# Kernel tuning notes

Hardware: AMD Instinct MI355X
Metric: run time of the kernel (lower is better)

The kernel has to match this reference:

```python
import jax, jax.numpy as jnp
import numpy as np

B, N, DEG = 128, 512, 8          # graphs, nodes per graph, avg degree
E = B * N * DEG                  # 524288 edges
F_IN, H1, H2, C = 128, 64, 128, 10
RATIO = 0.8
K = int(np.ceil(RATIO * N))      # TopKPooling keeps ceil(0.8*N)=410 nodes per graph


def setup_inputs() -> dict:
    key = jax.random.key(0)
    ks = jax.random.split(key, 10)
    n_nodes = B * N
    x = jax.random.normal(ks[0], (n_nodes, F_IN), dtype=jnp.float32)
    # random intra-graph edges, then offset node ids per graph
    src = jax.random.randint(ks[1], (B, N * DEG), 0, N)
    dst = jax.random.randint(ks[2], (B, N * DEG), 0, N)
    off = (jnp.arange(B) * N)[:, None]
    edge_index = jnp.stack([(src + off).reshape(-1), (dst + off).reshape(-1)]).astype(jnp.int64)
    batch = jnp.repeat(jnp.arange(B), N).astype(jnp.int64)
    s1 = 1.0 / np.sqrt(F_IN)
    s2 = 1.0 / np.sqrt(H1)
    s3 = 1.0 / np.sqrt(H2)
    return {
        "x": x,
        "edge_index": edge_index,
        "batch": batch,
        "W1": jax.random.uniform(ks[3], (F_IN, H1), jnp.float32, -s1, s1),
        "b1": jnp.zeros((H1,), jnp.float32),
        "W2": jax.random.uniform(ks[4], (H1, H2), jnp.float32, -s2, s2),
        "b2": jnp.zeros((H2,), jnp.float32),
        "pool_w": jax.random.uniform(ks[5], (H2,), jnp.float32, -s3, s3),
        "fc_W": jax.random.uniform(ks[6], (H2, C), jnp.float32, -s3, s3),
        "fc_b": jax.random.uniform(ks[7], (C,), jnp.float32, -s3, s3),
    }


def gcn_conv(x, W, b, src, dst, num_nodes):
    # PyG GCNConv: add self-loops, symmetric normalization, scatter-add aggregation
    loop = jnp.arange(num_nodes)
    src = jnp.concatenate([src, loop])
    dst = jnp.concatenate([dst, loop])
    deg = jax.ops.segment_sum(jnp.ones_like(src, dtype=x.dtype), dst, num_segments=num_nodes)
    dis = jnp.where(deg > 0, jax.lax.rsqrt(jnp.maximum(deg, 1.0)), 0.0)
    norm = dis[src] * dis[dst]                       # [E+N]
    h = x @ W                                        # transform first (smaller of the two in conv1)
    out = jax.ops.segment_sum(norm[:, None] * h[src], dst, num_segments=num_nodes)
    return out + b


def reference(x, edge_index, batch, W1, b1, W2, b2, pool_w, fc_W, fc_b):
    num_nodes = x.shape[0]
    src, dst = edge_index[0], edge_index[1]
    x = jax.nn.relu(gcn_conv(x, W1, b1, src, dst, num_nodes))
    x = jax.nn.relu(gcn_conv(x, W2, b2, src, dst, num_nodes))
    # TopKPooling: score = (x . w)/||w||, per-graph top-k on raw score, gate by tanh(score)
    score = (x @ pool_w) / jnp.linalg.norm(pool_w)   # [B*N]
    score_b = score.reshape(B, N)
    top_vals, top_idx = jax.lax.top_k(score_b, K)    # [B, K]
    x_b = x.reshape(B, N, H2)
    x_sel = jnp.take_along_axis(x_b, top_idx[:, :, None], axis=1)   # [B, K, H2]
    x_sel = x_sel * jnp.tanh(top_vals)[:, :, None]
    # global max pool over each (pooled) graph; pooled edge_index is unused downstream
    g = jnp.max(x_sel, axis=1)                        # [B, H2]
    logits = g @ fc_W + fc_b                          # [B, C]
    return jax.nn.log_softmax(logits, axis=1)
```

## Files before the change

kernel.cpp:

```cpp
#include <hip/hip_runtime.h>
#include <hip/hip_bf16.h>


#define BB 128
#define NN 512
#define NODES (BB*NN)
#define EE (BB*NN*8)
#define EDGPG (NN*8)
#define F_IN 128
#define H1 64
#define H2 128
#define NC 10
#define KSEL 410
#define EPG (NN*8 + NN)
#define TOT_ADJ (EE + NODES)

typedef unsigned short u16;
typedef unsigned int   u32;

static __device__ __forceinline__ float lo2f(u32 u){ return __uint_as_float(u << 16); }
static __device__ __forceinline__ float hi2f(u32 u){ return __uint_as_float(u & 0xffff0000u); }
static __device__ __forceinline__ u16 f2b(float f){
    __hip_bfloat16 h = __float2bfloat16(f);
    return *reinterpret_cast<u16*>(&h);
}
static __device__ __forceinline__ u32 packbf(float a, float b){
    return (u32)f2b(a) | ((u32)f2b(b) << 16);
}
static __device__ __forceinline__ void acc8(float* a, uint4 v){
    a[0] += lo2f(v.x); a[1] += hi2f(v.x);
    a[2] += lo2f(v.y); a[3] += hi2f(v.y);
    a[4] += lo2f(v.z); a[5] += hi2f(v.z);
    a[6] += lo2f(v.w); a[7] += hi2f(v.w);
}

static __device__ __forceinline__ bool ei_is_i64(const int* __restrict__ ei){
    return ((ei[1] | ei[3] | ei[5] | ei[7]) == 0);
}
static __device__ __forceinline__ int ld_src(const int* __restrict__ ei, int e, bool w64){
    return w64 ? ei[2*e] : ei[e];
}
static __device__ __forceinline__ int ld_dst(const int* __restrict__ ei, int e, bool w64){
    return w64 ? ei[2*(EE + e)] : ei[EE + e];
}

__global__ __launch_bounds__(512) void k_build(const int* __restrict__ ei,
                                               int* __restrict__ row_start,
                                               int* __restrict__ cnt_g,
                                               float* __restrict__ dis,
                                               int* __restrict__ adj){
    __shared__ int cnt[NN];
    __shared__ int sh[NN];
    __shared__ int cur[NN];
    __shared__ u16 ldst[EDGPG];
    bool w64 = ei_is_i64(ei);
    int b = blockIdx.x, t = threadIdx.x;
    cnt[t] = 0;
    __syncthreads();
    int e0 = b*EDGPG;
    for (int i = t; i < EDGPG; i += 512){
        int d = (ld_dst(ei, e0 + i, w64) - b*NN) & (NN - 1);
        ldst[i] = (u16)d;
        atomicAdd(&cnt[d], 1);
    }
    __syncthreads();
    int tot = cnt[t] + 1;
    sh[t] = tot;
    __syncthreads();
    for (int off = 1; off < NN; off <<= 1){
        int v = (t >= off) ? sh[t-off] : 0;
        __syncthreads();
        sh[t] += v;
        __syncthreads();
    }
    int rs_local = sh[t] - tot;
    row_start[b*NN + t] = b*EPG + rs_local;
    cnt_g[b*NN + t]     = tot - 1;
    dis[b*NN + t]       = rsqrtf((float)tot);
    cur[t] = rs_local;
    __syncthreads();
    {
        int p = atomicAdd(&cur[t], 1);
        adj[b*EPG + p] = b*NN + t;
    }
    for (int i = t; i < EDGPG; i += 512){
        int d = (int)ldst[i];
        int s = ld_src(ei, e0 + i, w64) & (NODES - 1);
        int p = atomicAdd(&cur[d], 1);
        adj[b*EPG + p] = s;
    }
}

#define G1NODES 64
#define XPAD 68
__global__ __launch_bounds__(256) void k_gemm1(const float* __restrict__ x,
                                               const float* __restrict__ W1,
                                               const float* __restrict__ dis,
                                               u32* __restrict__ h1u){
    __shared__ __align__(16) float Ws[64*H1];
    __shared__ __align__(16) float xs[G1NODES*XPAD];
    int t = threadIdx.x;
    int node0 = blockIdx.x*G1NODES;
    int tc = t & 15, tr = t >> 4;
    int j0 = tc*4, n0 = tr*4;
    float acc[4][4] = {};
    for (int half = 0; half < 2; ++half){
        const float4* Wv = (const float4*)(W1 + half*4096);
        for (int i = t; i < 1024; i += 256)
            *(float4*)&Ws[i*4] = Wv[i];
        for (int i = t; i < 1024; i += 256){
            int node = i >> 4, c = i & 15;
            float4 v = *(const float4*)(x + (size_t)(node0 + node)*F_IN + half*64 + c*4);
            *(float4*)&xs[node*XPAD + c*4] = v;
        }
        __syncthreads();
        #pragma unroll 2
        for (int k = 0; k < 64; k += 4){
            float4 xv0 = *(const float4*)&xs[(n0+0)*XPAD + k];
            float4 xv1 = *(const float4*)&xs[(n0+1)*XPAD + k];
            float4 xv2 = *(const float4*)&xs[(n0+2)*XPAD + k];
            float4 xv3 = *(const float4*)&xs[(n0+3)*XPAD + k];
            float xa0[4] = {xv0.x, xv0.y, xv0.z, xv0.w};
            float xa1[4] = {xv1.x, xv1.y, xv1.z, xv1.w};
            float xa2[4] = {xv2.x, xv2.y, xv2.z, xv2.w};
            float xa3[4] = {xv3.x, xv3.y, xv3.z, xv3.w};
            #pragma unroll
            for (int kk = 0; kk < 4; ++kk){
                float4 wv = *(const float4*)&Ws[(k+kk)*H1 + j0];
                acc[0][0] += xa0[kk]*wv.x; acc[0][1] += xa0[kk]*wv.y; acc[0][2] += xa0[kk]*wv.z; acc[0][3] += xa0[kk]*wv.w;
                acc[1][0] += xa1[kk]*wv.x; acc[1][1] += xa1[kk]*wv.y; acc[1][2] += xa1[kk]*wv.z; acc[1][3] += xa1[kk]*wv.w;
                acc[2][0] += xa2[kk]*wv.x; acc[2][1] += xa2[kk]*wv.y; acc[2][2] += xa2[kk]*wv.z; acc[2][3] += xa2[kk]*wv.w;
                acc[3][0] += xa3[kk]*wv.x; acc[3][1] += xa3[kk]*wv.y; acc[3][2] += xa3[kk]*wv.z; acc[3][3] += xa3[kk]*wv.w;
            }
        }
        __syncthreads();
    }
    #pragma unroll
    for (int i = 0; i < 4; ++i){
        float dn = dis[node0 + n0 + i];
        size_t base = (size_t)(node0 + n0 + i)*32 + tc*2;
        h1u[base]     = packbf(dn*acc[i][0], dn*acc[i][1]);
        h1u[base + 1] = packbf(dn*acc[i][2], dn*acc[i][3]);
    }
}

__global__ __launch_bounds__(256) void k_agg1(const uint4* __restrict__ h1v,
                                              const int* __restrict__ row_start,
                                              const int* __restrict__ cnt,
                                              const int* __restrict__ adj,
                                              const float* __restrict__ dis,
                                              const float4* __restrict__ b1v,
                                              uint4* __restrict__ a1v){
    int t = threadIdx.x;
    int node = blockIdx.x*32 + (t >> 3);
    int fl = t & 7;
    int rs = row_start[node];
    int deg = cnt[node] + 1; if (deg > EPG) deg = EPG;
    int pe = rs + deg;
    float a0[8] = {}, a1r[8] = {}, a2r[8] = {}, a3r[8] = {};
    int p = rs;
    for (; p + 4 <= pe; p += 4){
        int s0 = adj[p], s1 = adj[p+1], s2 = adj[p+2], s3 = adj[p+3];
        uint4 v0 = h1v[s0*8 + fl];
        uint4 v1 = h1v[s1*8 + fl];
        uint4 v2 = h1v[s2*8 + fl];
        uint4 v3 = h1v[s3*8 + fl];
        acc8(a0, v0); acc8(a1r, v1); acc8(a2r, v2); acc8(a3r, v3);
    }
    for (; p < pe; ++p){
        uint4 v = h1v[adj[p]*8 + fl];
        acc8(a0, v);
    }
    float r[8];
    #pragma unroll
    for (int j = 0; j < 8; ++j) r[j] = (a0[j] + a1r[j]) + (a2r[j] + a3r[j]);
    float dn = dis[node];
    float4 bA = b1v[2*fl], bB = b1v[2*fl+1];
    float w0 = dn*r[0] + bA.x; w0 = w0 > 0.f ? w0 : 0.f;
    float w1 = dn*r[1] + bA.y; w1 = w1 > 0.f ? w1 : 0.f;
    float w2 = dn*r[2] + bA.z; w2 = w2 > 0.f ? w2 : 0.f;
    float w3 = dn*r[3] + bA.w; w3 = w3 > 0.f ? w3 : 0.f;
    float w4 = dn*r[4] + bB.x; w4 = w4 > 0.f ? w4 : 0.f;
    float w5 = dn*r[5] + bB.y; w5 = w5 > 0.f ? w5 : 0.f;
    float w6 = dn*r[6] + bB.z; w6 = w6 > 0.f ? w6 : 0.f;
    float w7 = dn*r[7] + bB.w; w7 = w7 > 0.f ? w7 : 0.f;
    a1v[node*8 + fl] = make_uint4(packbf(dn*w0, dn*w1), packbf(dn*w2, dn*w3),
                                  packbf(dn*w4, dn*w5), packbf(dn*w6, dn*w7));
}

#define G2NODES 32
#define APAD 68
__global__ __launch_bounds__(256) void k_gemm2s(const uint4* __restrict__ a1v,
                                                const int* __restrict__ row_start,
                                                const int* __restrict__ cnt,
                                                const int* __restrict__ adj,
                                                const float* __restrict__ dis,
                                                const float* __restrict__ W2,
                                                const float* __restrict__ b2,
                                                const float* __restrict__ pw,
                                                u32* __restrict__ a2u,
                                                float* __restrict__ score){
    __shared__ __align__(16) float Ws[32*H2];
    __shared__ __align__(16) float as[G2NODES*APAD];
    __shared__ float pws[H2];
    int t = threadIdx.x;
    int node0 = blockIdx.x*G2NODES;
    if (t < H2) pws[t] = pw[t];
    {
        int fl = t & 7, nl = t >> 3;
        int node = node0 + nl;
        int rs = row_start[node];
        int deg = cnt[node] + 1; if (deg > EPG) deg = EPG;
        int pe = rs + deg;
        float a0[8] = {}, a1r[8] = {}, a2r[8] = {}, a3r[8] = {};
        int p = rs;
        for (; p + 4 <= pe; p += 4){
            int s0 = adj[p], s1 = adj[p+1], s2 = adj[p+2], s3 = adj[p+3];
            uint4 v0 = a1v[s0*8 + fl];
            uint4 v1 = a1v[s1*8 + fl];
            uint4 v2 = a1v[s2*8 + fl];
            uint4 v3 = a1v[s3*8 + fl];
            acc8(a0, v0); acc8(a1r, v1); acc8(a2r, v2); acc8(a3r, v3);
        }
        for (; p < pe; ++p){
            uint4 v = a1v[adj[p]*8 + fl];
            acc8(a0, v);
        }
        float dn = dis[node];
        float* dst = &as[nl*APAD + 8*fl];
        float r0 = dn*((a0[0] + a1r[0]) + (a2r[0] + a3r[0]));
        float r1 = dn*((a0[1] + a1r[1]) + (a2r[1] + a3r[1]));
        float r2 = dn*((a0[2] + a1r[2]) + (a2r[2] + a3r[2]));
        float r3 = dn*((a0[3] + a1r[3]) + (a2r[3] + a3r[3]));
        float r4 = dn*((a0[4] + a1r[4]) + (a2r[4] + a3r[4]));
        float r5 = dn*((a0[5] + a1r[5]) + (a2r[5] + a3r[5]));
        float r6 = dn*((a0[6] + a1r[6]) + (a2r[6] + a3r[6]));
        float r7 = dn*((a0[7] + a1r[7]) + (a2r[7] + a3r[7]));
        *(float4*)&dst[0] = make_float4(r0, r1, r2, r3);
        *(float4*)&dst[4] = make_float4(r4, r5, r6, r7);
    }
    int tc = t & 31, tr = t >> 5;
    int j0 = tc*4, n0 = tr*4;
    float acc[4][4] = {};
    for (int half = 0; half < 2; ++half){
        const float4* Wv = (const float4*)(W2 + half*4096);
        for (int i = t; i < 1024; i += 256)
            *(float4*)&Ws[i*4] = Wv[i];
        __syncthreads();
        int kb = half*32;
        #pragma unroll 2
        for (int k = 0; k < 32; k += 4){
            float4 xv0 = *(const float4*)&as[(n0+0)*APAD + kb + k];
            float4 xv1 = *(const float4*)&as[(n0+1)*APAD + kb + k];
            float4 xv2 = *(const float4*)&as[(n0+2)*APAD + kb + k];
            float4 xv3 = *(const float4*)&as[(n0+3)*APAD + kb + k];
            float xa0[4] = {xv0.x, xv0.y, xv0.z, xv0.w};
            float xa1[4] = {xv1.x, xv1.y, xv1.z, xv1.w};
            float xa2[4] = {xv2.x, xv2.y, xv2.z, xv2.w};
            float xa3[4] = {xv3.x, xv3.y, xv3.z, xv3.w};
            #pragma unroll
            for (int kk = 0; kk < 4; ++kk){
                float4 wv = *(const float4*)&Ws[(k+kk)*H2 + j0];
                acc[0][0] += xa0[kk]*wv.x; acc[0][1] += xa0[kk]*wv.y; acc[0][2] += xa0[kk]*wv.z; acc[0][3] += xa0[kk]*wv.w;
                acc[1][0] += xa1[kk]*wv.x; acc[1][1] += xa1[kk]*wv.y; acc[1][2] += xa1[kk]*wv.z; acc[1][3] += xa1[kk]*wv.w;
                acc[2][0] += xa2[kk]*wv.x; acc[2][1] += xa2[kk]*wv.y; acc[2][2] += xa2[kk]*wv.z; acc[2][3] += xa2[kk]*wv.w;
                acc[3][0] += xa3[kk]*wv.x; acc[3][1] += xa3[kk]*wv.y; acc[3][2] += xa3[kk]*wv.z; acc[3][3] += xa3[kk]*wv.w;
            }
        }
        __syncthreads();
    }
    float p0 = pws[j0], p1 = pws[j0+1], p2 = pws[j0+2], p3 = pws[j0+3];
    float bj0 = b2[j0], bj1 = b2[j0+1], bj2 = b2[j0+2], bj3 = b2[j0+3];
    #pragma unroll
    for (int i = 0; i < 4; ++i){
        float v0 = acc[i][0] + bj0; v0 = v0 > 0.f ? v0 : 0.f;
        float v1 = acc[i][1] + bj1; v1 = v1 > 0.f ? v1 : 0.f;
        float v2 = acc[i][2] + bj2; v2 = v2 > 0.f ? v2 : 0.f;
        float v3 = acc[i][3] + bj3; v3 = v3 > 0.f ? v3 : 0.f;
        size_t base = (size_t)(node0 + n0 + i)*64 + tc*2;
        a2u[base]     = packbf(v0, v1);
        a2u[base + 1] = packbf(v2, v3);
        float sp = v0*p0 + v1*p1 + v2*p2 + v3*p3;
        sp += __shfl_xor(sp, 16, 32);
        sp += __shfl_xor(sp,  8, 32);
        sp += __shfl_xor(sp,  4, 32);
        sp += __shfl_xor(sp,  2, 32);
        sp += __shfl_xor(sp,  1, 32);
        if (tc == 0) score[node0 + n0 + i] = sp;
    }
}

__global__ __launch_bounds__(512) void k_pool(const u32* __restrict__ a2u,
                                              const float* __restrict__ score,
                                              const float* __restrict__ pw,
                                              const float* __restrict__ fcW,
                                              const float* __restrict__ fcb,
                                              float* __restrict__ out){
    __shared__ float so[NN];
    __shared__ float ss[NN];
    __shared__ float th[NN];
    __shared__ float pm[32*H2];
    __shared__ float gl[H2];
    __shared__ float fws[H2*NC];
    __shared__ float lg[NC];
    __shared__ float red[3];
    int b = blockIdx.x, t = threadIdx.x;
    for (int i = t; i < H2*NC; i += 512) fws[i] = fcW[i];
    if (t < H2){ float v = pw[t]; gl[t] = v*v; }
    __syncthreads();
    if (t == 0){
        float s = 0.f;
        for (int i = 0; i < H2; ++i) s += gl[i];
        red[2] = rsqrtf(s);
    }
    __syncthreads();
    float pwinv = red[2];
    float sc = score[b*NN + t];
    so[t] = sc; ss[t] = sc; th[t] = tanhf(sc*pwinv);
    __syncthreads();
    for (int k = 2; k <= NN; k <<= 1){
        for (int j = k >> 1; j > 0; j >>= 1){
            int ixj = t ^ j;
            if (ixj > t){
                float a = ss[t], c = ss[ixj];
                bool desc = ((t & k) == 0);
                bool sw = desc ? (a < c) : (a > c);
                if (sw){ ss[t] = c; ss[ixj] = a; }
            }
            __syncthreads();
        }
    }
    float thresh = ss[KSEL-1];
    float mask_t = (so[t] >= thresh) ? 0.f : -INFINITY;
    __syncthreads();
    so[t] = mask_t;
    __syncthreads();
    int tc = t & 15, q = t >> 4;
    const uint4* ap = (const uint4*)(a2u + (size_t)b*NN*64);
    float m0 = -INFINITY, m1 = -INFINITY, m2 = -INFINITY, m3 = -INFINITY;
    float m4 = -INFINITY, m5 = -INFINITY, m6 = -INFINITY, m7 = -INFINITY;
    int nb = q*16;
    #pragma unroll 4
    for (int n = nb; n < nb + 16; ++n){
        uint4 v = ap[(size_t)n*16 + tc];
        float thn = th[n], son = so[n];
        m0 = fmaxf(m0, lo2f(v.x)*thn + son);
        m1 = fmaxf(m1, hi2f(v.x)*thn + son);
        m2 = fmaxf(m2, lo2f(v.y)*thn + son);
        m3 = fmaxf(m3, hi2f(v.y)*thn + son);
        m4 = fmaxf(m4, lo2f(v.z)*thn + son);
        m5 = fmaxf(m5, hi2f(v.z)*thn + son);
        m6 = fmaxf(m6, lo2f(v.w)*thn + son);
        m7 = fmaxf(m7, hi2f(v.w)*thn + son);
    }
    float* pmr = &pm[q*H2 + 8*tc];
    pmr[0] = m0; pmr[1] = m1; pmr[2] = m2; pmr[3] = m3;
    pmr[4] = m4; pmr[5] = m5; pmr[6] = m6; pmr[7] = m7;
    __syncthreads();
    if (t < H2){
        float g = pm[t];
        #pragma unroll
        for (int qq = 1; qq < 32; ++qq) g = fmaxf(g, pm[qq*H2 + t]);
        gl[t] = g;
    }
    __syncthreads();
    if (t < NC){
        float acc = fcb[t];
        for (int k2 = 0; k2 < H2; ++k2) acc += gl[k2]*fws[k2*NC + t];
        lg[t] = acc;
    }
    __syncthreads();
    if (t == 0){
        float mx = lg[0];
        for (int i = 1; i < NC; ++i) mx = fmaxf(mx, lg[i]);
        float s = 0.f;
        for (int i = 0; i < NC; ++i) s += expf(lg[i] - mx);
        red[0] = mx; red[1] = logf(s);
    }
    __syncthreads();
    if (t < NC) out[b*NC + t] = lg[t] - red[0] - red[1];
}

extern "C" void kernel_launch(void* const* d_in, const int* in_sizes, int n_in,
                              void* d_out, int out_size, void* d_ws, size_t ws_size,
                              hipStream_t stream) {
    const float* x   = (const float*)d_in[0];
    const int*   ei  = (const int*)d_in[1];
    const float* W1  = (const float*)d_in[3];
    const float* b1  = (const float*)d_in[4];
    const float* W2  = (const float*)d_in[5];
    const float* b2  = (const float*)d_in[6];
    const float* pw  = (const float*)d_in[7];
    const float* fcW = (const float*)d_in[8];
    const float* fcb = (const float*)d_in[9];

    char* ws = (char*)d_ws;
    int*   cnt       = (int*)(ws + 4096);
    int*   row_start = (int*)(ws + 266240);
    float* dis       = (float*)(ws + 528384);
    float* score     = (float*)(ws + 790528);
    int*   adj       = (int*)(ws + 1052672);
    u32*   h1u       = (u32*)(ws + 4194304);
    u32*   a1u       = (u32*)(ws + 12582912);
    u32*   a2u       = (u32*)(ws + 20971520);

    k_build<<<BB, 512, 0, stream>>>(ei, row_start, cnt, dis, adj);
    k_gemm1<<<NODES/G1NODES, 256, 0, stream>>>(x, W1, dis, h1u);
    k_agg1<<<NODES/32, 256, 0, stream>>>((const uint4*)h1u, row_start, cnt, adj, dis,
                                         (const float4*)b1, (uint4*)a1u);
    k_gemm2s<<<NODES/G2NODES, 256, 0, stream>>>((const uint4*)a1u, row_start, cnt, adj,
                                                dis, W2, b2, pw, a2u, score);
    k_pool<<<BB, 512, 0, stream>>>(a2u, score, pw, fcW, fcb, (float*)d_out);
}
```

Measured before the change: 176.3 us.

## Fuse graph build with GEMM1 and pooling into GEMM2 via last-block counter

Merges the CSR build and first GEMM into one launch: the GEMM blocks recompute per-node degree from edge destinations themselves, so they need not wait for the build. The pooling/top-k/classifier stage is folded into the second GEMM kernel; the last of the 16 blocks covering a graph, detected with an atomic done counter and threadfences, runs the pooling for that graph with 256 threads. This removes two kernel launches and their inter-kernel gaps, at the cost of redundant edge scans in GEMM1 blocks and a serialized tail for pooling.

```diff
diff --git a/kernel.cpp b/kernel.cpp
--- a/kernel.cpp
+++ b/kernel.cpp
@@ -44,89 +44,110 @@
     return w64 ? ei[2*(EE + e)] : ei[EE + e];
 }
 
-__global__ __launch_bounds__(512) void k_build(const int* __restrict__ ei,
-                                               int* __restrict__ row_start,
-                                               int* __restrict__ cnt_g,
-                                               float* __restrict__ dis,
-                                               int* __restrict__ adj){
-    __shared__ int cnt[NN];
-    __shared__ int sh[NN];
-    __shared__ int cur[NN];
-    __shared__ u16 ldst[EDGPG];
+#define G1NODES 128
+#define XPAD 68
+#define G1BLOCKS (NODES/G1NODES)
+
+union SM1 {
+    struct { int cnt[NN]; int sh[NN]; int cur[NN]; u16 ldst[EDGPG]; } b;
+    struct { float Ws[64*H1]; float xs[G1NODES*XPAD]; int degs[G1NODES]; } g;
+};
+
+__global__ __launch_bounds__(512) void k_build_gemm1(const int* __restrict__ ei,
+                                                     const float* __restrict__ x,
+                                                     const float* __restrict__ W1,
+                                                     int* __restrict__ row_start,
+                                                     int* __restrict__ cnt_g,
+                                                     float* __restrict__ dis,
+                                                     int* __restrict__ adj,
+                                                     u32* __restrict__ h1u,
+                                                     int* __restrict__ done){
+    __shared__ SM1 sm;
     bool w64 = ei_is_i64(ei);
-    int b = blockIdx.x, t = threadIdx.x;
-    cnt[t] = 0;
-    __syncthreads();
-    int e0 = b*EDGPG;
-    for (int i = t; i < EDGPG; i += 512){
-        int d = (ld_dst(ei, e0 + i, w64) - b*NN) & (NN - 1);
-        ldst[i] = (u16)d;
-        atomicAdd(&cnt[d], 1);
-    }
-    __syncthreads();
-    int tot = cnt[t] + 1;
-    sh[t] = tot;
-    __syncthreads();
-    for (int off = 1; off < NN; off <<= 1){
-        int v = (t >= off) ? sh[t-off] : 0;
-        __syncthreads();
-        sh[t] += v;
-        __syncthreads();
-    }
-    int rs_local = sh[t] - tot;
-    row_start[b*NN + t] = b*EPG + rs_local;
-    cnt_g[b*NN + t]     = tot - 1;
-    dis[b*NN + t]       = rsqrtf((float)tot);
-    cur[t] = rs_local;
-    __syncthreads();
-    {
-        int p = atomicAdd(&cur[t], 1);
-        adj[b*EPG + p] = b*NN + t;
-    }
-    for (int i = t; i < EDGPG; i += 512){
-        int d = (int)ldst[i];
-        int s = ld_src(ei, e0 + i, w64) & (NODES - 1);
-        int p = atomicAdd(&cur[d], 1);
-        adj[b*EPG + p] = s;
-    }
-}
-
-#define G1NODES 64
-#define XPAD 68
-__global__ __launch_bounds__(256) void k_gemm1(const float* __restrict__ x,
-                                               const float* __restrict__ W1,
-                                               const float* __restrict__ dis,
-                                               u32* __restrict__ h1u){
-    __shared__ __align__(16) float Ws[64*H1];
-    __shared__ __align__(16) float xs[G1NODES*XPAD];
     int t = threadIdx.x;
-    int node0 = blockIdx.x*G1NODES;
+
+    if (blockIdx.x < BB){
+        int b = blockIdx.x;
+        if (t == 0) done[b] = 0;
+        sm.b.cnt[t] = 0;
+        __syncthreads();
+        int e0 = b*EDGPG;
+        for (int i = t; i < EDGPG; i += 512){
+            int d = (ld_dst(ei, e0 + i, w64) - b*NN) & (NN - 1);
+            sm.b.ldst[i] = (u16)d;
+            atomicAdd(&sm.b.cnt[d], 1);
+        }
+        __syncthreads();
+        int tot = sm.b.cnt[t] + 1;
+        sm.b.sh[t] = tot;
+        __syncthreads();
+        for (int off = 1; off < NN; off <<= 1){
+            int v = (t >= off) ? sm.b.sh[t-off] : 0;
+            __syncthreads();
+            sm.b.sh[t] += v;
+            __syncthreads();
+        }
+        int rs_local = sm.b.sh[t] - tot;
+        row_start[b*NN + t] = b*EPG + rs_local;
+        cnt_g[b*NN + t]     = tot - 1;
+        dis[b*NN + t]       = rsqrtf((float)tot);
+        sm.b.cur[t] = rs_local;
+        __syncthreads();
+        {
+            int p = atomicAdd(&sm.b.cur[t], 1);
+            adj[b*EPG + p] = b*NN + t;
+        }
+        for (int i = t; i < EDGPG; i += 512){
+            int d = (int)sm.b.ldst[i];
+            int s = ld_src(ei, e0 + i, w64) & (NODES - 1);
+            int p = atomicAdd(&sm.b.cur[d], 1);
+            adj[b*EPG + p] = s;
+        }
+        return;
+    }
+
+    int gb = (int)blockIdx.x - BB;
+    int b  = gb >> 2;
+    int nloc0 = (gb & 3) * G1NODES;
+    int node0 = b*NN + nloc0;
     int tc = t & 15, tr = t >> 4;
     int j0 = tc*4, n0 = tr*4;
+
+    if (t < G1NODES) sm.g.degs[t] = 0;
+    __syncthreads();
+    {
+        int e0 = b*EDGPG;
+        for (int i = t; i < EDGPG; i += 512){
+            int d = (ld_dst(ei, e0 + i, w64) - b*NN) & (NN - 1);
+            unsigned r = (unsigned)(d - nloc0);
+            if (r < G1NODES) atomicAdd(&sm.g.degs[r], 1);
+        }
+    }
+
     float acc[4][4] = {};
     for (int half = 0; half < 2; ++half){
         const float4* Wv = (const float4*)(W1 + half*4096);
-        for (int i = t; i < 1024; i += 256)
-            *(float4*)&Ws[i*4] = Wv[i];
-        for (int i = t; i < 1024; i += 256){
+        for (int i = t; i < 1024; i += 512)
+            *(float4*)&sm.g.Ws[i*4] = Wv[i];
+        for (int i = t; i < 2048; i += 512){
             int node = i >> 4, c = i & 15;
             float4 v = *(const float4*)(x + (size_t)(node0 + node)*F_IN + half*64 + c*4);
-            *(float4*)&xs[node*XPAD + c*4] = v;
+            *(float4*)&sm.g.xs[node*XPAD + c*4] = v;
         }
         __syncthreads();
         #pragma unroll 2
         for (int k = 0; k < 64; k += 4){
-            float4 xv0 = *(const float4*)&xs[(n0+0)*XPAD + k];
-            float4 xv1 = *(const float4*)&xs[(n0+1)*XPAD + k];
-            float4 xv2 = *(const float4*)&xs[(n0+2)*XPAD + k];
-            float4 xv3 = *(const float4*)&xs[(n0+3)*XPAD + k];
+            float4 xv0 = *(const float4*)&sm.g.xs[(n0+0)*XPAD + k];
+            float4 xv1 = *(const float4*)&sm.g.xs[(n0+1)*XPAD + k];
+            float4 xv2 = *(const float4*)&sm.g.xs[(n0+2)*XPAD + k];
+            float4 xv3 = *(const float4*)&sm.g.xs[(n0+3)*XPAD + k];
             float xa0[4] = {xv0.x, xv0.y, xv0.z, xv0.w};
             float xa1[4] = {xv1.x, xv1.y, xv1.z, xv1.w};
             float xa2[4] = {xv2.x, xv2.y, xv2.z, xv2.w};
             float xa3[4] = {xv3.x, xv3.y, xv3.z, xv3.w};
             #pragma unroll
             for (int kk = 0; kk < 4; ++kk){
-                float4 wv = *(const float4*)&Ws[(k+kk)*H1 + j0];
+                float4 wv = *(const float4*)&sm.g.Ws[(k+kk)*H1 + j0];
                 acc[0][0] += xa0[kk]*wv.x; acc[0][1] += xa0[kk]*wv.y; acc[0][2] += xa0[kk]*wv.z; acc[0][3] += xa0[kk]*wv.w;
                 acc[1][0] += xa1[kk]*wv.x; acc[1][1] += xa1[kk]*wv.y; acc[1][2] += xa1[kk]*wv.z; acc[1][3] += xa1[kk]*wv.w;
                 acc[2][0] += xa2[kk]*wv.x; acc[2][1] += xa2[kk]*wv.y; acc[2][2] += xa2[kk]*wv.z; acc[2][3] += xa2[kk]*wv.w;
@@ -137,7 +158,7 @@
     }
     #pragma unroll
     for (int i = 0; i < 4; ++i){
-        float dn = dis[node0 + n0 + i];
+        float dn = rsqrtf((float)(sm.g.degs[n0 + i] + 1));
         size_t base = (size_t)(node0 + n0 + i)*32 + tc*2;
         h1u[base]     = packbf(dn*acc[i][0], dn*acc[i][1]);
         h1u[base + 1] = packbf(dn*acc[i][2], dn*acc[i][3]);
@@ -190,22 +211,32 @@
 
 #define G2NODES 32
 #define APAD 68
-__global__ __launch_bounds__(256) void k_gemm2s(const uint4* __restrict__ a1v,
-                                                const int* __restrict__ row_start,
-                                                const int* __restrict__ cnt,
-                                                const int* __restrict__ adj,
-                                                const float* __restrict__ dis,
-                                                const float* __restrict__ W2,
-                                                const float* __restrict__ b2,
-                                                const float* __restrict__ pw,
-                                                u32* __restrict__ a2u,
-                                                float* __restrict__ score){
-    __shared__ __align__(16) float Ws[32*H2];
-    __shared__ __align__(16) float as[G2NODES*APAD];
-    __shared__ float pws[H2];
+
+union SM3 {
+    struct { float Ws[32*H2]; float as[G2NODES*APAD]; float pws[H2]; } g;
+    struct { float ss[NN]; float so[NN]; float th[NN]; float pm[16*H2];
+             float gl[H2]; float fws[H2*NC]; float lg[NC]; float red[4]; } p;
+};
+
+__global__ __launch_bounds__(256) void k_gemm2sp(const uint4* __restrict__ a1v,
+                                                 const int* __restrict__ row_start,
+                                                 const int* __restrict__ cnt,
+                                                 const int* __restrict__ adj,
+                                                 const float* __restrict__ dis,
+                                                 const float* __restrict__ W2,
+                                                 const float* __restrict__ b2,
+                                                 const float* __restrict__ pw,
+                                                 const float* __restrict__ fcW,
+                                                 const float* __restrict__ fcb,
+                                                 u32* __restrict__ a2u,
+                                                 float* __restrict__ score,
+                                                 int* __restrict__ done,
+                                                 float* __restrict__ out){
+    __shared__ SM3 sm;
+    __shared__ int win;
     int t = threadIdx.x;
     int node0 = blockIdx.x*G2NODES;
-    if (t < H2) pws[t] = pw[t];
+    if (t < H2) sm.g.pws[t] = pw[t];
     {
         int fl = t & 7, nl = t >> 3;
         int node = node0 + nl;
@@ -227,7 +258,7 @@
             acc8(a0, v);
         }
         float dn = dis[node];
-        float* dst = &as[nl*APAD + 8*fl];
+        float* dst = &sm.g.as[nl*APAD + 8*fl];
         float r0 = dn*((a0[0] + a1r[0]) + (a2r[0] + a3r[0]));
         float r1 = dn*((a0[1] + a1r[1]) + (a2r[1] + a3r[1]));
         float r2 = dn*((a0[2] + a1r[2]) + (a2r[2] + a3r[2]));
@@ -245,22 +276,22 @@
     for (int half = 0; half < 2; ++half){
         const float4* Wv = (const float4*)(W2 + half*4096);
         for (int i = t; i < 1024; i += 256)
-            *(float4*)&Ws[i*4] = Wv[i];
+            *(float4*)&sm.g.Ws[i*4] = Wv[i];
         __syncthreads();
         int kb = half*32;
         #pragma unroll 2
         for (int k = 0; k < 32; k += 4){
-            float4 xv0 = *(const float4*)&as[(n0+0)*APAD + kb + k];
-            float4 xv1 = *(const float4*)&as[(n0+1)*APAD + kb + k];
-            float4 xv2 = *(const float4*)&as[(n0+2)*APAD + kb + k];
-            float4 xv3 = *(const float4*)&as[(n0+3)*APAD + kb + k];
+            float4 xv0 = *(const float4*)&sm.g.as[(n0+0)*APAD + kb + k];
+            float4 xv1 = *(const float4*)&sm.g.as[(n0+1)*APAD + kb + k];
+            float4 xv2 = *(const float4*)&sm.g.as[(n0+2)*APAD + kb + k];
+            float4 xv3 = *(const float4*)&sm.g.as[(n0+3)*APAD + kb + k];
             float xa0[4] = {xv0.x, xv0.y, xv0.z, xv0.w};
             float xa1[4] = {xv1.x, xv1.y, xv1.z, xv1.w};
             float xa2[4] = {xv2.x, xv2.y, xv2.z, xv2.w};
             float xa3[4] = {xv3.x, xv3.y, xv3.z, xv3.w};
             #pragma unroll
             for (int kk = 0; kk < 4; ++kk){
-                float4 wv = *(const float4*)&Ws[(k+kk)*H2 + j0];
+                float4 wv = *(const float4*)&sm.g.Ws[(k+kk)*H2 + j0];
                 acc[0][0] += xa0[kk]*wv.x; acc[0][1] += xa0[kk]*wv.y; acc[0][2] += xa0[kk]*wv.z; acc[0][3] += xa0[kk]*wv.w;
                 acc[1][0] += xa1[kk]*wv.x; acc[1][1] += xa1[kk]*wv.y; acc[1][2] += xa1[kk]*wv.z; acc[1][3] += xa1[kk]*wv.w;
                 acc[2][0] += xa2[kk]*wv.x; acc[2][1] += xa2[kk]*wv.y; acc[2][2] += xa2[kk]*wv.z; acc[2][3] += xa2[kk]*wv.w;
@@ -269,7 +300,7 @@
         }
         __syncthreads();
     }
-    float p0 = pws[j0], p1 = pws[j0+1], p2 = pws[j0+2], p3 = pws[j0+3];
+    float p0 = sm.g.pws[j0], p1 = sm.g.pws[j0+1], p2 = sm.g.pws[j0+2], p3 = sm.g.pws[j0+3];
     float bj0 = b2[j0], bj1 = b2[j0+1], bj2 = b2[j0+2], bj3 = b2[j0+3];
     #pragma unroll
     for (int i = 0; i < 4; ++i){
@@ -288,97 +319,93 @@
         sp += __shfl_xor(sp,  1, 32);
         if (tc == 0) score[node0 + n0 + i] = sp;
     }
-}
-
-__global__ __launch_bounds__(512) void k_pool(const u32* __restrict__ a2u,
-                                              const float* __restrict__ score,
-                                              const float* __restrict__ pw,
-                                              const float* __restrict__ fcW,
-                                              const float* __restrict__ fcb,
-                                              float* __restrict__ out){
-    __shared__ float so[NN];
-    __shared__ float ss[NN];
-    __shared__ float th[NN];
-    __shared__ float pm[32*H2];
-    __shared__ float gl[H2];
-    __shared__ float fws[H2*NC];
-    __shared__ float lg[NC];
-    __shared__ float red[3];
-    int b = blockIdx.x, t = threadIdx.x;
-    for (int i = t; i < H2*NC; i += 512) fws[i] = fcW[i];
-    if (t < H2){ float v = pw[t]; gl[t] = v*v; }
+
+    int b = blockIdx.x >> 4;
+    __syncthreads();
+    if (t == 0){
+        __threadfence();
+        win = (atomicAdd(&done[b], 1) == 15);
+    }
+    __syncthreads();
+    if (!win) return;
+    __threadfence();
+
+    for (int i = t; i < H2*NC; i += 256) sm.p.fws[i] = fcW[i];
+    if (t < H2){ float v = pw[t]; sm.p.gl[t] = v*v; }
     __syncthreads();
     if (t == 0){
         float s = 0.f;
-        for (int i = 0; i < H2; ++i) s += gl[i];
-        red[2] = rsqrtf(s);
-    }
-    __syncthreads();
-    float pwinv = red[2];
-    float sc = score[b*NN + t];
-    so[t] = sc; ss[t] = sc; th[t] = tanhf(sc*pwinv);
+        for (int i = 0; i < H2; ++i) s += sm.p.gl[i];
+        sm.p.red[2] = rsqrtf(s);
+    }
+    __syncthreads();
+    float pwinv = sm.p.red[2];
+    for (int i = t; i < NN; i += 256){
+        float sc = score[b*NN + i];
+        sm.p.so[i] = sc; sm.p.ss[i] = sc; sm.p.th[i] = tanhf(sc*pwinv);
+    }
     __syncthreads();
     for (int k = 2; k <= NN; k <<= 1){
         for (int j = k >> 1; j > 0; j >>= 1){
-            int ixj = t ^ j;
-            if (ixj > t){
-                float a = ss[t], c = ss[ixj];
-                bool desc = ((t & k) == 0);
-                bool sw = desc ? (a < c) : (a > c);
-                if (sw){ ss[t] = c; ss[ixj] = a; }
-            }
+            int i   = ((t & ~(j-1)) << 1) | (t & (j-1));
+            int ixj = i | j;
+            float a = sm.p.ss[i], c = sm.p.ss[ixj];
+            bool desc = ((i & k) == 0);
+            bool sw = desc ? (a < c) : (a > c);
+            if (sw){ sm.p.ss[i] = c; sm.p.ss[ixj] = a; }
             __syncthreads();
         }
     }
-    float thresh = ss[KSEL-1];
-    float mask_t = (so[t] >= thresh) ? 0.f : -INFINITY;
-    __syncthreads();
-    so[t] = mask_t;
-    __syncthreads();
-    int tc = t & 15, q = t >> 4;
-    const uint4* ap = (const uint4*)(a2u + (size_t)b*NN*64);
-    float m0 = -INFINITY, m1 = -INFINITY, m2 = -INFINITY, m3 = -INFINITY;
-    float m4 = -INFINITY, m5 = -INFINITY, m6 = -INFINITY, m7 = -INFINITY;
-    int nb = q*16;
-    #pragma unroll 4
-    for (int n = nb; n < nb + 16; ++n){
-        uint4 v = ap[(size_t)n*16 + tc];
-        float thn = th[n], son = so[n];
-        m0 = fmaxf(m0, lo2f(v.x)*thn + son);
-        m1 = fmaxf(m1, hi2f(v.x)*thn + son);
-        m2 = fmaxf(m2, lo2f(v.y)*thn + son);
-        m3 = fmaxf(m3, hi2f(v.y)*thn + son);
-        m4 = fmaxf(m4, lo2f(v.z)*thn + son);
-        m5 = fmaxf(m5, hi2f(v.z)*thn + son);
-        m6 = fmaxf(m6, lo2f(v.w)*thn + son);
-        m7 = fmaxf(m7, hi2f(v.w)*thn + son);
-    }
-    float* pmr = &pm[q*H2 + 8*tc];
-    pmr[0] = m0; pmr[1] = m1; pmr[2] = m2; pmr[3] = m3;
-    pmr[4] = m4; pmr[5] = m5; pmr[6] = m6; pmr[7] = m7;
+    float thresh = sm.p.ss[KSEL-1];
+    for (int i = t; i < NN; i += 256)
+        sm.p.so[i] = (sm.p.so[i] >= thresh) ? 0.f : -INFINITY;
+    __syncthreads();
+    {
+        int pc = t & 15, q = t >> 4;
+        const uint4* ap = (const uint4*)(a2u + (size_t)b*NN*64);
+        float m0 = -INFINITY, m1 = -INFINITY, m2 = -INFINITY, m3 = -INFINITY;
+        float m4 = -INFINITY, m5 = -INFINITY, m6 = -INFINITY, m7 = -INFINITY;
+        int nb = q*32;
+        #pragma unroll 4
+        for (int n = nb; n < nb + 32; ++n){
+            uint4 v = ap[(size_t)n*16 + pc];
+            float thn = sm.p.th[n], son = sm.p.so[n];
+            m0 = fmaxf(m0, lo2f(v.x)*thn + son);
+            m1 = fmaxf(m1, hi2f(v.x)*thn + son);
+            m2 = fmaxf(m2, lo2f(v.y)*thn + son);
+            m3 = fmaxf(m3, hi2f(v.y)*thn + son);
+            m4 = fmaxf(m4, lo2f(v.z)*thn + son);
+            m5 = fmaxf(m5, hi2f(v.z)*thn + son);
+            m6 = fmaxf(m6, lo2f(v.w)*thn + son);
+            m7 = fmaxf(m7, hi2f(v.w)*thn + son);
+        }
+        float* pmr = &sm.p.pm[q*H2 + 8*pc];
+        pmr[0] = m0; pmr[1] = m1; pmr[2] = m2; pmr[3] = m3;
+        pmr[4] = m4; pmr[5] = m5; pmr[6] = m6; pmr[7] = m7;
+    }
     __syncthreads();
     if (t < H2){
-        float g = pm[t];
+        float g = sm.p.pm[t];
         #pragma unroll
-        for (int qq = 1; qq < 32; ++qq) g = fmaxf(g, pm[qq*H2 + t]);
-        gl[t] = g;
+        for (int qq = 1; qq < 16; ++qq) g = fmaxf(g, sm.p.pm[qq*H2 + t]);
+        sm.p.gl[t] = g;
     }
     __syncthreads();
     if (t < NC){
-        float acc = fcb[t];
-        for (int k2 = 0; k2 < H2; ++k2) acc += gl[k2]*fws[k2*NC + t];
-        lg[t] = acc;
+        float acc2 = fcb[t];
+        for (int k2 = 0; k2 < H2; ++k2) acc2 += sm.p.gl[k2]*sm.p.fws[k2*NC + t];
+        sm.p.lg[t] = acc2;
     }
     __syncthreads();
     if (t == 0){
-        float mx = lg[0];
-        for (int i = 1; i < NC; ++i) mx = fmaxf(mx, lg[i]);
+        float mx = sm.p.lg[0];
+        for (int i = 1; i < NC; ++i) mx = fmaxf(mx, sm.p.lg[i]);
         float s = 0.f;
-        for (int i = 0; i < NC; ++i) s += expf(lg[i] - mx);
-        red[0] = mx; red[1] = logf(s);
-    }
-    __syncthreads();
-    if (t < NC) out[b*NC + t] = lg[t] - red[0] - red[1];
+        for (int i = 0; i < NC; ++i) s += expf(sm.p.lg[i] - mx);
+        sm.p.red[0] = mx; sm.p.red[1] = logf(s);
+    }
+    __syncthreads();
+    if (t < NC) out[b*NC + t] = sm.p.lg[t] - sm.p.red[0] - sm.p.red[1];
 }
 
 extern "C" void kernel_launch(void* const* d_in, const int* in_sizes, int n_in,
@@ -395,6 +422,7 @@
     const float* fcb = (const float*)d_in[9];
 
     char* ws = (char*)d_ws;
+    int*   done      = (int*)(ws + 0);
     int*   cnt       = (int*)(ws + 4096);
     int*   row_start = (int*)(ws + 266240);
     float* dis       = (float*)(ws + 528384);
@@ -404,11 +432,11 @@
     u32*   a1u       = (u32*)(ws + 12582912);
     u32*   a2u       = (u32*)(ws + 20971520);
 
-    k_build<<<BB, 512, 0, stream>>>(ei, row_start, cnt, dis, adj);
-    k_gemm1<<<NODES/G1NODES, 256, 0, stream>>>(x, W1, dis, h1u);
+    k_build_gemm1<<<BB + G1BLOCKS, 512, 0, stream>>>(ei, x, W1, row_start, cnt, dis,
+                                                     adj, h1u, done);
     k_agg1<<<NODES/32, 256, 0, stream>>>((const uint4*)h1u, row_start, cnt, adj, dis,
                                          (const float4*)b1, (uint4*)a1u);
-    k_gemm2s<<<NODES/G2NODES, 256, 0, stream>>>((const uint4*)a1u, row_start, cnt, adj,
-                                                dis, W2, b2, pw, a2u, score);
-    k_pool<<<BB, 512, 0, stream>>>(a2u, score, pw, fcW, fcb, (float*)d_out);
-}
+    k_gemm2sp<<<NODES/G2NODES, 256, 0, stream>>>((const uint4*)a1u, row_start, cnt, adj,
+                                                 dis, W2, b2, pw, fcW, fcb,
+                                                 a2u, score, done, (float*)d_out);
+}
```

Result: slower. 339.6 us (+92.6%).

## Fuse CSR build with first GEMM and swizzle aggregation block order

Applied to the files above, without the earlier changes.

Merges the adjacency build kernel and the first GEMM into a single launch. The first 128 blocks build the CSR, and the remaining blocks each process 128 nodes and recompute in-degrees locally from edge_index, so they no longer wait for the dis array. This removes one launch and lets the serial per-graph build run alongside the GEMM, at the cost of every GEMM block rescanning its graph's edges. It also swizzles block indices in both aggregation kernels (blockIdx mod 8 placed in the high bits), likely to spread consecutive node ranges across XCD L2 caches.

```diff
diff --git a/kernel.cpp b/kernel.cpp
--- a/kernel.cpp
+++ b/kernel.cpp
@@ -33,6 +33,9 @@
     a[4] += lo2f(v.z); a[5] += hi2f(v.z);
     a[6] += lo2f(v.w); a[7] += hi2f(v.w);
 }
+static __device__ __forceinline__ int swz2048(int bid){
+    return ((bid & 7) << 8) | (bid >> 3);
+}
 
 static __device__ __forceinline__ bool ei_is_i64(const int* __restrict__ ei){
     return ((ei[1] | ei[3] | ei[5] | ei[7]) == 0);
@@ -44,89 +47,108 @@
     return w64 ? ei[2*(EE + e)] : ei[EE + e];
 }
 
-__global__ __launch_bounds__(512) void k_build(const int* __restrict__ ei,
-                                               int* __restrict__ row_start,
-                                               int* __restrict__ cnt_g,
-                                               float* __restrict__ dis,
-                                               int* __restrict__ adj){
-    __shared__ int cnt[NN];
-    __shared__ int sh[NN];
-    __shared__ int cur[NN];
-    __shared__ u16 ldst[EDGPG];
+#define G1NODES 128
+#define XPAD 68
+#define G1BLOCKS (NODES/G1NODES)
+
+union SM1 {
+    struct { int cnt[NN]; int sh[NN]; int cur[NN]; u16 ldst[EDGPG]; } b;
+    struct { float Ws[64*H1]; float xs[G1NODES*XPAD]; int degs[G1NODES]; } g;
+};
+
+__global__ __launch_bounds__(512) void k_build_gemm1(const int* __restrict__ ei,
+                                                     const float* __restrict__ x,
+                                                     const float* __restrict__ W1,
+                                                     int* __restrict__ row_start,
+                                                     int* __restrict__ cnt_g,
+                                                     float* __restrict__ dis,
+                                                     int* __restrict__ adj,
+                                                     u32* __restrict__ h1u){
+    __shared__ SM1 sm;
     bool w64 = ei_is_i64(ei);
-    int b = blockIdx.x, t = threadIdx.x;
-    cnt[t] = 0;
-    __syncthreads();
-    int e0 = b*EDGPG;
-    for (int i = t; i < EDGPG; i += 512){
-        int d = (ld_dst(ei, e0 + i, w64) - b*NN) & (NN - 1);
-        ldst[i] = (u16)d;
-        atomicAdd(&cnt[d], 1);
-    }
-    __syncthreads();
-    int tot = cnt[t] + 1;
-    sh[t] = tot;
-    __syncthreads();
-    for (int off = 1; off < NN; off <<= 1){
-        int v = (t >= off) ? sh[t-off] : 0;
-        __syncthreads();
-        sh[t] += v;
-        __syncthreads();
-    }
-    int rs_local = sh[t] - tot;
-    row_start[b*NN + t] = b*EPG + rs_local;
-    cnt_g[b*NN + t]     = tot - 1;
-    dis[b*NN + t]       = rsqrtf((float)tot);
-    cur[t] = rs_local;
-    __syncthreads();
-    {
-        int p = atomicAdd(&cur[t], 1);
-        adj[b*EPG + p] = b*NN + t;
-    }
-    for (int i = t; i < EDGPG; i += 512){
-        int d = (int)ldst[i];
-        int s = ld_src(ei, e0 + i, w64) & (NODES - 1);
-        int p = atomicAdd(&cur[d], 1);
-        adj[b*EPG + p] = s;
-    }
-}
-
-#define G1NODES 64
-#define XPAD 68
-__global__ __launch_bounds__(256) void k_gemm1(const float* __restrict__ x,
-                                               const float* __restrict__ W1,
-                                               const float* __restrict__ dis,
-                                               u32* __restrict__ h1u){
-    __shared__ __align__(16) float Ws[64*H1];
-    __shared__ __align__(16) float xs[G1NODES*XPAD];
     int t = threadIdx.x;
-    int node0 = blockIdx.x*G1NODES;
+
+    if (blockIdx.x < BB){
+        int b = blockIdx.x;
+        sm.b.cnt[t] = 0;
+        __syncthreads();
+        int e0 = b*EDGPG;
+        for (int i = t; i < EDGPG; i += 512){
+            int d = (ld_dst(ei, e0 + i, w64) - b*NN) & (NN - 1);
+            sm.b.ldst[i] = (u16)d;
+            atomicAdd(&sm.b.cnt[d], 1);
+        }
+        __syncthreads();
+        int tot = sm.b.cnt[t] + 1;
+        sm.b.sh[t] = tot;
+        __syncthreads();
+        for (int off = 1; off < NN; off <<= 1){
+            int v = (t >= off) ? sm.b.sh[t-off] : 0;
+            __syncthreads();
+            sm.b.sh[t] += v;
+            __syncthreads();
+        }
+        int rs_local = sm.b.sh[t] - tot;
+        row_start[b*NN + t] = b*EPG + rs_local;
+        cnt_g[b*NN + t]     = tot - 1;
+        dis[b*NN + t]       = rsqrtf((float)tot);
+        sm.b.cur[t] = rs_local;
+        __syncthreads();
+        {
+            int p = atomicAdd(&sm.b.cur[t], 1);
+            adj[b*EPG + p] = b*NN + t;
+        }
+        for (int i = t; i < EDGPG; i += 512){
+            int d = (int)sm.b.ldst[i];
+            int s = ld_src(ei, e0 + i, w64) & (NODES - 1);
+            int p = atomicAdd(&sm.b.cur[d], 1);
+            adj[b*EPG + p] = s;
+        }
+        return;
+    }
+
+    int gb = (int)blockIdx.x - BB;
+    int b  = gb >> 2;
+    int nloc0 = (gb & 3) * G1NODES;
+    int node0 = b*NN + nloc0;
     int tc = t & 15, tr = t >> 4;
     int j0 = tc*4, n0 = tr*4;
+
+    if (t < G1NODES) sm.g.degs[t] = 0;
+    __syncthreads();
+    {
+        int e0 = b*EDGPG;
+        for (int i = t; i < EDGPG; i += 512){
+            int d = (ld_dst(ei, e0 + i, w64) - b*NN) & (NN - 1);
+            unsigned r = (unsigned)(d - nloc0);
+            if (r < G1NODES) atomicAdd(&sm.g.degs[r], 1);
+        }
+    }
+
     float acc[4][4] = {};
     for (int half = 0; half < 2; ++half){
         const float4* Wv = (const float4*)(W1 + half*4096);
-        for (int i = t; i < 1024; i += 256)
-            *(float4*)&Ws[i*4] = Wv[i];
-        for (int i = t; i < 1024; i += 256){
+        for (int i = t; i < 1024; i += 512)
+            *(float4*)&sm.g.Ws[i*4] = Wv[i];
+        for (int i = t; i < 2048; i += 512){
             int node = i >> 4, c = i & 15;
             float4 v = *(const float4*)(x + (size_t)(node0 + node)*F_IN + half*64 + c*4);
-            *(float4*)&xs[node*XPAD + c*4] = v;
+            *(float4*)&sm.g.xs[node*XPAD + c*4] = v;
         }
         __syncthreads();
         #pragma unroll 2
         for (int k = 0; k < 64; k += 4){
-            float4 xv0 = *(const float4*)&xs[(n0+0)*XPAD + k];
-            float4 xv1 = *(const float4*)&xs[(n0+1)*XPAD + k];
-            float4 xv2 = *(const float4*)&xs[(n0+2)*XPAD + k];
-            float4 xv3 = *(const float4*)&xs[(n0+3)*XPAD + k];
+            float4 xv0 = *(const float4*)&sm.g.xs[(n0+0)*XPAD + k];
+            float4 xv1 = *(const float4*)&sm.g.xs[(n0+1)*XPAD + k];
+            float4 xv2 = *(const float4*)&sm.g.xs[(n0+2)*XPAD + k];
+            float4 xv3 = *(const float4*)&sm.g.xs[(n0+3)*XPAD + k];
             float xa0[4] = {xv0.x, xv0.y, xv0.z, xv0.w};
             float xa1[4] = {xv1.x, xv1.y, xv1.z, xv1.w};
             float xa2[4] = {xv2.x, xv2.y, xv2.z, xv2.w};
             float xa3[4] = {xv3.x, xv3.y, xv3.z, xv3.w};
             #pragma unroll
             for (int kk = 0; kk < 4; ++kk){
-                float4 wv = *(const float4*)&Ws[(k+kk)*H1 + j0];
+                float4 wv = *(const float4*)&sm.g.Ws[(k+kk)*H1 + j0];
                 acc[0][0] += xa0[kk]*wv.x; acc[0][1] += xa0[kk]*wv.y; acc[0][2] += xa0[kk]*wv.z; acc[0][3] += xa0[kk]*wv.w;
                 acc[1][0] += xa1[kk]*wv.x; acc[1][1] += xa1[kk]*wv.y; acc[1][2] += xa1[kk]*wv.z; acc[1][3] += xa1[kk]*wv.w;
                 acc[2][0] += xa2[kk]*wv.x; acc[2][1] += xa2[kk]*wv.y; acc[2][2] += xa2[kk]*wv.z; acc[2][3] += xa2[kk]*wv.w;
@@ -137,7 +159,7 @@
     }
     #pragma unroll
     for (int i = 0; i < 4; ++i){
-        float dn = dis[node0 + n0 + i];
+        float dn = rsqrtf((float)(sm.g.degs[n0 + i] + 1));
         size_t base = (size_t)(node0 + n0 + i)*32 + tc*2;
         h1u[base]     = packbf(dn*acc[i][0], dn*acc[i][1]);
         h1u[base + 1] = packbf(dn*acc[i][2], dn*acc[i][3]);
@@ -152,7 +174,8 @@
                                               const float4* __restrict__ b1v,
                                               uint4* __restrict__ a1v){
     int t = threadIdx.x;
-    int node = blockIdx.x*32 + (t >> 3);
+    int lb = swz2048((int)blockIdx.x);
+    int node = lb*32 + (t >> 3);
     int fl = t & 7;
     int rs = row_start[node];
     int deg = cnt[node] + 1; if (deg > EPG) deg = EPG;
@@ -204,7 +227,8 @@
     __shared__ __align__(16) float as[G2NODES*APAD];
     __shared__ float pws[H2];
     int t = threadIdx.x;
-    int node0 = blockIdx.x*G2NODES;
+    int lb = swz2048((int)blockIdx.x);
+    int node0 = lb*G2NODES;
     if (t < H2) pws[t] = pw[t];
     {
         int fl = t & 7, nl = t >> 3;
@@ -404,8 +428,8 @@
     u32*   a1u       = (u32*)(ws + 12582912);
     u32*   a2u       = (u32*)(ws + 20971520);
 
-    k_build<<<BB, 512, 0, stream>>>(ei, row_start, cnt, dis, adj);
-    k_gemm1<<<NODES/G1NODES, 256, 0, stream>>>(x, W1, dis, h1u);
+    k_build_gemm1<<<BB + G1BLOCKS, 512, 0, stream>>>(ei, x, W1, row_start, cnt, dis,
+                                                     adj, h1u);
     k_agg1<<<NODES/32, 256, 0, stream>>>((const uint4*)h1u, row_start, cnt, adj, dis,
                                          (const float4*)b1, (uint4*)a1u);
     k_gemm2s<<<NODES/G2NODES, 256, 0, stream>>>((const uint4*)a1u, row_start, cnt, adj,
```

Measured after the change: 174.5 us. Within noise of the previous version (-1.0%).
